# Kernel tuning notes

Hardware: AMD Instinct MI355X
Metric: run time of the kernel (lower is better)

## Reference

```python
import jax, jax.numpy as jnp
import numpy as np

EPS = 1e-5
K = 16
D = 2

def _bn(x, gamma, beta):
    # eval-mode BatchNorm with running_mean=0, running_var=1
    return x * (gamma / jnp.sqrt(1.0 + EPS)) + beta

def _dense(x, W, b, gamma=None, beta=None, act=True):
    y = x @ W + b
    if act:
        y = jax.nn.elu(y)
    if gamma is not None:
        y = _bn(y, gamma, beta)
    return y

def setup_inputs() -> dict:
    key = jax.random.key(0)
    ks = jax.random.split(key, 16)
    N, Npts, P, dims = 16, 8192, 2048, 3
    C_in, C_out = 64, 128
    C_mid = C_out // 4      # 32
    C_half = C_out // 2     # 64
    dm = 2                  # depth_multiplier = min(ceil(C_out/C_in), 4)
    Ccat = C_mid + C_half   # 96
    def w(k, shape, fan_in):
        return (jax.random.normal(k, shape, jnp.float32) / np.float32(np.sqrt(fan_in)))
    return {
        "rep_pts": jax.random.normal(ks[0], (N, P, dims), jnp.float32),
        "pts": jax.random.normal(ks[1], (N, Npts, dims), jnp.float32),
        "fts": jax.random.normal(ks[2], (N, Npts, C_in), jnp.float32),
        "pts_idx": jax.random.randint(ks[3], (N, P, K * D), 0, Npts),
        # PointCNN.dense: C_in -> C_out//2 (Linear+ELU+BN)
        "dense_W": w(ks[4], (C_in, C_half), C_in), "dense_b": jnp.zeros(C_half),
        "dense_g": jnp.ones(C_half), "dense_bt": jnp.zeros(C_half),
        # XConv dense1/dense2: dims->C_mid->C_mid
        "d1_W": w(ks[5], (dims, C_mid), dims), "d1_b": jnp.zeros(C_mid),
        "d1_g": jnp.ones(C_mid), "d1_bt": jnp.zeros(C_mid),
        "d2_W": w(ks[6], (C_mid, C_mid), C_mid), "d2_b": jnp.zeros(C_mid),
        "d2_g": jnp.ones(C_mid), "d2_bt": jnp.zeros(C_mid),
        "xt_cW": w(ks[7], (K * K, dims, K), dims * K), "xt_cb": jnp.zeros(K * K),
        "xt_d1W": w(ks[8], (K * K, K * K), K * K), "xt_d1b": jnp.zeros(K * K),
        "xt_d2W": w(ks[9], (K * K, K * K), K * K), "xt_d2b": jnp.zeros(K * K),
        # end_conv SepConv: depthwise (1,K) with depth_multiplier, then pointwise 1x1
        "dw_W": w(ks[10], (Ccat, dm, K), K), "dw_b": jnp.zeros(Ccat * dm),
        "pw_W": w(ks[11], (Ccat * dm, C_out), Ccat * dm), "pw_b": jnp.zeros(C_out),
        "sep_g": jnp.ones(C_out), "sep_bt": jnp.zeros(C_out),
    }

def reference(rep_pts, pts, fts, pts_idx,
              dense_W, dense_b, dense_g, dense_bt,
              d1_W, d1_b, d1_g, d1_bt,
              d2_W, d2_b, d2_g, d2_bt,
              xt_cW, xt_cb, xt_d1W, xt_d1b, xt_d2W, xt_d2b,
              dw_W, dw_b, pw_W, pw_b, sep_g, sep_bt):
    idx = pts_idx[:, :, : K * D : D]                  # [N,P,K]
    gather = jax.vmap(lambda a, i: a[i])              # per-batch neighbor gather
    # fts -> Dense(C_in, C_out//2)
    fts_l = _dense(fts, dense_W, dense_b, dense_g, dense_bt)
    pts_reg = gather(pts, idx)                        # [N,P,K,dims]
    fts_reg = gather(fts_l, idx)                      # [N,P,K,C_half]
    pts_local = pts_reg - rep_pts[:, :, None, :]      # center neighborhoods
    # lift coordinates to C_mid features
    l0 = _dense(pts_local, d1_W, d1_b, d1_g, d1_bt)
    lifted = _dense(l0, d2_W, d2_b, d2_g, d2_bt)      # [N,P,K,C_mid]
    fts_cat = jnp.concatenate([lifted, fts_reg], axis=-1)  # [N,P,K,Ccat]
    # X-transform: Conv (1,K) over dims -> K*K (ELU, no BN), two Dense (last no act)
    Xc = jax.nn.elu(jnp.einsum('npkd,odk->npo', pts_local, xt_cW) + xt_cb)
    X = jax.nn.elu(Xc @ xt_d1W + xt_d1b)
    X = X @ xt_d2W + xt_d2b
    N_, P_ = X.shape[0], X.shape[1]
    X = X.reshape(N_, P_, K, K)
    fts_X = jnp.einsum('npij,npjc->npic', X, fts_cat)  # [N,P,K,Ccat]
    # depthwise separable conv over K, then ELU + BN, squeeze -> [N,P,C_out]
    dw = jnp.einsum('npkc,cmk->npcm', fts_X, dw_W).reshape(N_, P_, -1) + dw_b
    out = jax.nn.elu(dw @ pw_W + pw_b)
    out = _bn(out, sep_g, sep_bt)
    return out
```

## Files before the change

### kernel.cpp

```cpp
#include <hip/hip_runtime.h>
#include <hip/hip_bf16.h>

#define RS 0.9999950000374998f

__device__ __forceinline__ float eluf(float x) {
    return x > 0.0f ? x : __expf(x) - 1.0f;
}

typedef __attribute__((ext_vector_type(8))) __bf16 bf16x8;
typedef __attribute__((ext_vector_type(4))) float f32x4;
typedef __attribute__((ext_vector_type(4))) unsigned int u32x4;

__global__ __launch_bounds__(256) void gather_kernel(
    const float* __restrict__ rep_pts, const float* __restrict__ pts,
    const int* __restrict__ pts_idx, const float* __restrict__ d1W,
    const float* __restrict__ d2W, const float* __restrict__ pwW,
    const float* __restrict__ d2Ws, const float* __restrict__ denseW,
    const float* __restrict__ cW, float* __restrict__ pts_local,
    __hip_bfloat16* __restrict__ PLB, __hip_bfloat16* __restrict__ d1Wt,
    __hip_bfloat16* __restrict__ d2Wt, __hip_bfloat16* __restrict__ pwWt,
    __hip_bfloat16* __restrict__ d2pWt, __hip_bfloat16* __restrict__ denseWt,
    __hip_bfloat16* __restrict__ cWt) {
    const int tid = threadIdx.x;
    if (blockIdx.x < 256) {
        const int t = blockIdx.x * 256 + tid;
        {
            const int k = t >> 8, n = t & 255;
            d1Wt[n * 256 + k] = __float2bfloat16(d1W[t]);
            d2Wt[n * 256 + k] = __float2bfloat16(d2W[t]);
        }
        if (t < 24576) {
            const int k = t >> 7, n = t & 127;
            pwWt[n * 192 + k] = __float2bfloat16(pwW[t]);
        }
        if (t < 1024) {
            const int q = t >> 5, c = t & 31;
            d2pWt[c * 32 + q] = __float2bfloat16(d2Ws[t]);
        }
        if (t < 4096) {
            const int k = t >> 6, n = t & 63;
            denseWt[n * 64 + k] = __float2bfloat16(denseW[t]);
        }
        if (t < 16384) {
            const int o = t >> 6, kq = t & 63;
            cWt[t] = (kq < 48) ? __float2bfloat16(cW[o * 48 + kq])
                               : __float2bfloat16(0.0f);
        }
    }
    const long gp0 = (long)blockIdx.x * 16;
    const int pt = tid >> 4, k = tid & 15;
    const long gp = gp0 + pt;
    const int n = (int)(gp >> 11);
    const int idx = pts_idx[gp * 32 + 2 * k];
    const float* ps = pts + ((long)n * 8192 + idx) * 3;
    const float* rs = rep_pts + gp * 3;
#pragma unroll
    for (int d = 0; d < 3; ++d) {
        const float v = ps[d] - rs[d];
        pts_local[gp * 48 + k * 3 + d] = v;
        PLB[gp * 64 + d * 16 + k] = __float2bfloat16(v);
    }
    PLB[gp * 64 + 48 + k] = __float2bfloat16(0.0f);
}

template <int TN, int ACT, int BN_, int OUTB>
__global__ __launch_bounds__(256) void mfma_gemm(
    const __hip_bfloat16* __restrict__ A, const __hip_bfloat16* __restrict__ Wt,
    const float* __restrict__ bias, const float* __restrict__ gamma,
    const float* __restrict__ beta, void* __restrict__ outp, int K, int Ncols) {
    constexpr int MT = (TN == 128) ? 4 : 2;
    constexpr int RB = MT * 16;
    __shared__ __bf16 As[128][40];
    __shared__ __bf16 Bs[TN][40];
    const int tid = threadIdx.x;
    const int w = tid >> 6, l = tid & 63;
    const int wm = (TN == 128) ? (w >> 1) : w;
    const int wn = (TN == 128) ? (w & 1) : 0;
    const long row0 = (long)blockIdx.x * 128;
    const int col0 = blockIdx.y * TN;
    const int sr = tid >> 1, sh = tid & 1;
    const int fr = l & 15, kg = (l >> 4) * 8;
    f32x4 acc[MT][4] = {};
    const __hip_bfloat16* __restrict__ ap = A + (row0 + sr) * (long)K + sh * 16;
    const __hip_bfloat16* __restrict__ bp =
        Wt + (long)(col0 + (TN == 128 ? sr : (sr & 63))) * K + sh * 16;
    for (int k0 = 0; k0 < K; k0 += 32) {
        const uint4 av0 = *reinterpret_cast<const uint4*>(ap + k0);
        const uint4 av1 = *reinterpret_cast<const uint4*>(ap + k0 + 8);
        *reinterpret_cast<uint4*>(&As[sr][sh * 16]) = av0;
        *reinterpret_cast<uint4*>(&As[sr][sh * 16 + 8]) = av1;
        if (TN == 128 || tid < 128) {
            const uint4 bv0 = *reinterpret_cast<const uint4*>(bp + k0);
            const uint4 bv1 = *reinterpret_cast<const uint4*>(bp + k0 + 8);
            *reinterpret_cast<uint4*>(&Bs[TN == 128 ? sr : (sr & 63)][sh * 16]) =
                bv0;
            *reinterpret_cast<uint4*>(
                &Bs[TN == 128 ? sr : (sr & 63)][sh * 16 + 8]) = bv1;
        }
        __syncthreads();
        bf16x8 af[MT], bfv[4];
#pragma unroll
        for (int mt = 0; mt < MT; ++mt)
            af[mt] =
                *reinterpret_cast<const bf16x8*>(&As[wm * RB + mt * 16 + fr][kg]);
#pragma unroll
        for (int nt = 0; nt < 4; ++nt)
            bfv[nt] =
                *reinterpret_cast<const bf16x8*>(&Bs[wn * 64 + nt * 16 + fr][kg]);
#pragma unroll
        for (int mt = 0; mt < MT; ++mt)
#pragma unroll
            for (int nt = 0; nt < 4; ++nt)
                acc[mt][nt] = __builtin_amdgcn_mfma_f32_16x16x32_bf16(
                    af[mt], bfv[nt], acc[mt][nt], 0, 0, 0);
        __syncthreads();
    }
    const int rg = (l >> 4) * 4;
#pragma unroll
    for (int nt = 0; nt < 4; ++nt) {
        const int col = col0 + wn * 64 + nt * 16 + fr;
        const float bb = bias[col];
        const float gs = BN_ ? gamma[col] * RS : 0.0f;
        const float bt = BN_ ? beta[col] : 0.0f;
#pragma unroll
        for (int mt = 0; mt < MT; ++mt) {
#pragma unroll
            for (int r = 0; r < 4; ++r) {
                const long row = row0 + wm * RB + mt * 16 + rg + r;
                float v = acc[mt][nt][r] + bb;
                if (ACT) v = eluf(v);
                if (BN_) v = v * gs + bt;
                if (OUTB)
                    reinterpret_cast<__hip_bfloat16*>(outp)[row * Ncols + col] =
                        __float2bfloat16(v);
                else
                    reinterpret_cast<float*>(outp)[row * Ncols + col] = v;
            }
        }
    }
}

__global__ __launch_bounds__(256) void mfma_gemm_f32a64(
    const float* __restrict__ A, const __hip_bfloat16* __restrict__ Wt,
    const float* __restrict__ bias, const float* __restrict__ gamma,
    const float* __restrict__ beta, __hip_bfloat16* __restrict__ outp, int K,
    int Ncols) {
    __shared__ __bf16 As[128][40];
    __shared__ __bf16 Bs[64][40];
    const int tid = threadIdx.x;
    const int w = tid >> 6, l = tid & 63;
    const long row0 = (long)blockIdx.x * 128;
    const int sr = tid >> 1, sh = tid & 1;
    const int fr = l & 15, kg = (l >> 4) * 8;
    f32x4 acc[2][4] = {};
    const float* __restrict__ ap = A + (row0 + sr) * (long)K + sh * 16;
    const __hip_bfloat16* __restrict__ bp = Wt + (long)(sr & 63) * K + sh * 16;
    for (int k0 = 0; k0 < K; k0 += 32) {
        float av[16];
#pragma unroll
        for (int q = 0; q < 4; ++q) {
            const float4 v = *reinterpret_cast<const float4*>(ap + k0 + q * 4);
            av[q * 4 + 0] = v.x;
            av[q * 4 + 1] = v.y;
            av[q * 4 + 2] = v.z;
            av[q * 4 + 3] = v.w;
        }
        union {
            __bf16 b[16];
            uint4 u[2];
        } cv;
#pragma unroll
        for (int e = 0; e < 16; ++e) cv.b[e] = (__bf16)av[e];
        *reinterpret_cast<uint4*>(&As[sr][sh * 16]) = cv.u[0];
        *reinterpret_cast<uint4*>(&As[sr][sh * 16 + 8]) = cv.u[1];
        if (tid < 128) {
            const uint4 bv0 = *reinterpret_cast<const uint4*>(bp + k0);
            const uint4 bv1 = *reinterpret_cast<const uint4*>(bp + k0 + 8);
            *reinterpret_cast<uint4*>(&Bs[sr & 63][sh * 16]) = bv0;
            *reinterpret_cast<uint4*>(&Bs[sr & 63][sh * 16 + 8]) = bv1;
        }
        __syncthreads();
        bf16x8 af[2], bfv[4];
#pragma unroll
        for (int mt = 0; mt < 2; ++mt)
            af[mt] =
                *reinterpret_cast<const bf16x8*>(&As[w * 32 + mt * 16 + fr][kg]);
#pragma unroll
        for (int nt = 0; nt < 4; ++nt)
            bfv[nt] = *reinterpret_cast<const bf16x8*>(&Bs[nt * 16 + fr][kg]);
#pragma unroll
        for (int mt = 0; mt < 2; ++mt)
#pragma unroll
            for (int nt = 0; nt < 4; ++nt)
                acc[mt][nt] = __builtin_amdgcn_mfma_f32_16x16x32_bf16(
                    af[mt], bfv[nt], acc[mt][nt], 0, 0, 0);
        __syncthreads();
    }
    const int rg = (l >> 4) * 4;
#pragma unroll
    for (int nt = 0; nt < 4; ++nt) {
        const int col = nt * 16 + fr;
        const float bb = bias[col];
        const float gs = gamma[col] * RS;
        const float bt = beta[col];
#pragma unroll
        for (int mt = 0; mt < 2; ++mt) {
#pragma unroll
            for (int r = 0; r < 4; ++r) {
                const long row = row0 + w * 32 + mt * 16 + rg + r;
                float v = acc[mt][nt][r] + bb;
                v = eluf(v) * gs + bt;
                outp[row * Ncols + col] = __float2bfloat16(v);
            }
        }
    }
}

__global__ __launch_bounds__(1024) void xchain_kernel(
    const __hip_bfloat16* __restrict__ PLB, const __hip_bfloat16* __restrict__ cWt,
    const float* __restrict__ cb, const __hip_bfloat16* __restrict__ d1Wt,
    const float* __restrict__ d1b, const __hip_bfloat16* __restrict__ d2Wt,
    const float* __restrict__ d2b, __hip_bfloat16* __restrict__ X2B) {
    __shared__ __bf16 Ap[128][264];
    __shared__ __bf16 Bs[256][40];
    const int tid = threadIdx.x;
    const int w = tid >> 6, l = tid & 63;
    const int wm = w >> 2, wn = w & 3;
    const long row0 = (long)blockIdx.x * 128;
    const int fr = l & 15, kg = (l >> 4) * 8, rg = (l >> 4) * 4;

    {
        const int r = tid >> 3, q = tid & 7;
        *reinterpret_cast<uint4*>(&Ap[r][q * 8]) =
            *reinterpret_cast<const uint4*>(PLB + (row0 + r) * 64 + q * 8);
    }
    __syncthreads();

    auto layer = [&](const __hip_bfloat16* __restrict__ Wt,
                     const float* __restrict__ bias, int K, bool act,
                     bool last) {
        f32x4 acc[2][4] = {};
        for (int k0 = 0; k0 < K; k0 += 32) {
            {
                const int col = tid >> 2, q = tid & 3;
                *reinterpret_cast<uint4*>(&Bs[col][q * 8]) =
                    *reinterpret_cast<const uint4*>(Wt + (long)col * K + k0 +
                                                    q * 8);
            }
            __syncthreads();
            bf16x8 af[2], bfv[4];
#pragma unroll
            for (int mt = 0; mt < 2; ++mt)
                af[mt] = *reinterpret_cast<const bf16x8*>(
                    &Ap[wm * 32 + mt * 16 + fr][k0 + kg]);
#pragma unroll
            for (int nt = 0; nt < 4; ++nt)
                bfv[nt] = *reinterpret_cast<const bf16x8*>(
                    &Bs[wn * 64 + nt * 16 + fr][kg]);
#pragma unroll
            for (int mt = 0; mt < 2; ++mt)
#pragma unroll
                for (int nt = 0; nt < 4; ++nt)
                    acc[mt][nt] = __builtin_amdgcn_mfma_f32_16x16x32_bf16(
                        af[mt], bfv[nt], acc[mt][nt], 0, 0, 0);
            __syncthreads();
        }
#pragma unroll
        for (int nt = 0; nt < 4; ++nt) {
            const int col = wn * 64 + nt * 16 + fr;
            const float bb = bias[col];
#pragma unroll
            for (int mt = 0; mt < 2; ++mt) {
#pragma unroll
                for (int r = 0; r < 4; ++r) {
                    const int row = wm * 32 + mt * 16 + rg + r;
                    float v = acc[mt][nt][r] + bb;
                    if (act) v = eluf(v);
                    const __bf16 h = (__bf16)v;
                    if (last)
                        X2B[(row0 + row) * 256 + col] =
                            *reinterpret_cast<const __hip_bfloat16*>(&h);
                    else
                        Ap[row][col] = h;
                }
            }
        }
        __syncthreads();
    };

    layer(cWt, cb, 64, true, false);
    layer(d1Wt, d1b, 256, true, false);
    layer(d2Wt, d2b, 256, false, true);
}

__global__ __launch_bounds__(1024) void final_stage_kernel(
    const __hip_bfloat16* __restrict__ X2B,
    const float* __restrict__ pts_local,
    const int* __restrict__ pts_idx,
    const __hip_bfloat16* __restrict__ fts_lB,
    const float* __restrict__ d1_W, const float* __restrict__ d1_b,
    const float* __restrict__ d1_g, const float* __restrict__ d1_bt,
    const __hip_bfloat16* __restrict__ d2pWt,
    const float* __restrict__ d2_b, const float* __restrict__ d2_g,
    const float* __restrict__ d2_bt, const float* __restrict__ dw_W,
    const float* __restrict__ dw_b,
    __hip_bfloat16* __restrict__ dw_out)
{
    __shared__ __bf16 fcat[16][96][16];
    __shared__ float dwT[96][36];
    __shared__ float wd1[6][32];
    __shared__ float d2e[3][32];
    __shared__ float dwbs[192];

    const int tid = threadIdx.x;
    const int w = tid >> 6, l = tid & 63;

    for (int i = tid; i < 3072; i += 1024) dwT[i >> 5][i & 31] = dw_W[i];
    if (tid < 96) wd1[tid >> 5][tid & 31] = d1_W[tid];
    else if (tid < 128) wd1[3][tid & 31] = d1_b[tid & 31];
    else if (tid < 160) wd1[4][tid & 31] = d1_g[tid & 31] * RS;
    else if (tid < 192) wd1[5][tid & 31] = d1_bt[tid & 31];
    else if (tid < 224) d2e[0][tid & 31] = d2_b[tid & 31];
    else if (tid < 256) d2e[1][tid & 31] = d2_g[tid & 31] * RS;
    else if (tid < 288) d2e[2][tid & 31] = d2_bt[tid & 31];
    else if (tid < 480) dwbs[tid - 288] = dw_b[tid - 288];
    __syncthreads();

    const int obid = blockIdx.x;
    const int bid = (obid & 7) * 256 + (obid >> 3);
    const int gp = bid * 16 + w;
    const int ugp = __builtin_amdgcn_readfirstlane(gp);
    const int n = ugp >> 11;
    const int fr = l & 15;
    const int kg = (l >> 4) * 8;
    const int kk = kg & 15;
    const unsigned msk = (l < 32) ? 0xFFFFFFFFu : 0u;
    const int rg4 = (l >> 4) * 4;
    const int colg = (l < 32) ? (32 + l) : (l - 32);
    const __hip_bfloat16* __restrict__ fbase =
        fts_lB + (long)n * 8192 * 64 + colg;

    const int* __restrict__ ip = pts_idx + (long)ugp * 32;
    unsigned fg[16];
#pragma unroll
    for (int j = 0; j < 16; ++j)
        fg[j] = *reinterpret_cast<const unsigned short*>(
            &fbase[(long)ip[2 * j] * 64]);

    const float* __restrict__ pp = pts_local + (long)ugp * 48 + fr * 3;
    const float plA0 = pp[0], plA1 = pp[1], plA2 = pp[2];

    bf16x8 a_l0;
#pragma unroll
    for (int jj = 0; jj < 8; ++jj) {
        const int q = kg + jj;
        float a = wd1[3][q];
        a = fmaf(plA0, wd1[0][q], a);
        a = fmaf(plA1, wd1[1][q], a);
        a = fmaf(plA2, wd1[2][q], a);
        a = eluf(a);
        a = a * wd1[4][q] + wd1[5][q];
        a_l0[jj] = (__bf16)a;
    }

    {
        const bf16x8 b0 =
            *reinterpret_cast<const bf16x8*>(d2pWt + (0 + fr) * 32 + kg);
        const bf16x8 b1 =
            *reinterpret_cast<const bf16x8*>(d2pWt + (16 + fr) * 32 + kg);
        f32x4 lif0 = {}, lif1 = {};
        lif0 = __builtin_amdgcn_mfma_f32_16x16x32_bf16(a_l0, b0, lif0, 0, 0, 0);
        lif1 = __builtin_amdgcn_mfma_f32_16x16x32_bf16(a_l0, b1, lif1, 0, 0, 0);
#pragma unroll
        for (int f = 0; f < 2; ++f) {
            const int c = f * 16 + fr;
            const float bb = d2e[0][c & 31], gs = d2e[1][c & 31],
                        bt = d2e[2][c & 31];
            const f32x4 dd = f ? lif1 : lif0;
            unsigned short pk[4];
#pragma unroll
            for (int r = 0; r < 4; ++r) {
                float v = dd[r] + bb;
                v = eluf(v) * gs + bt;
                const __bf16 h = (__bf16)v;
                pk[r] = *reinterpret_cast<const unsigned short*>(&h);
            }
            *reinterpret_cast<uint2*>(&fcat[w][c][rg4]) =
                make_uint2((unsigned)pk[0] | ((unsigned)pk[1] << 16),
                           (unsigned)pk[2] | ((unsigned)pk[3] << 16));
        }
    }

    {
        const uint4 lo = make_uint4(fg[0] | (fg[1] << 16), fg[2] | (fg[3] << 16),
                                    fg[4] | (fg[5] << 16), fg[6] | (fg[7] << 16));
        const uint4 hi =
            make_uint4(fg[8] | (fg[9] << 16), fg[10] | (fg[11] << 16),
                       fg[12] | (fg[13] << 16), fg[14] | (fg[15] << 16));
        *reinterpret_cast<uint4*>(&fcat[w][32 + colg][0]) = lo;
        *reinterpret_cast<uint4*>(&fcat[w][32 + colg][8]) = hi;
    }

    u32x4 axu =
        *reinterpret_cast<const u32x4*>(X2B + (long)ugp * 256 + fr * 16 + kk);
    axu &= msk;
    const bf16x8 ax = *reinterpret_cast<const bf16x8*>(&axu);

    f32x4 acc[6];
#pragma unroll
    for (int f = 0; f < 6; ++f) acc[f] = (f32x4){};
#pragma unroll
    for (int f = 0; f < 6; ++f) {
        u32x4 bu = *reinterpret_cast<const u32x4*>(&fcat[w][f * 16 + fr][kk]);
        bu &= msk;
        const bf16x8 bf = *reinterpret_cast<const bf16x8*>(&bu);
        acc[f] = __builtin_amdgcn_mfma_f32_16x16x32_bf16(ax, bf, acc[f], 0, 0, 0);
    }

    float dwv[6][2];
#pragma unroll
    for (int f = 0; f < 6; ++f) {
        const int c = f * 16 + fr;
        const float4 w0 = *reinterpret_cast<const float4*>(&dwT[c][rg4]);
        const float4 w1 = *reinterpret_cast<const float4*>(&dwT[c][16 + rg4]);
        float p0 = acc[f][0] * w0.x;
        p0 = fmaf(acc[f][1], w0.y, p0);
        p0 = fmaf(acc[f][2], w0.z, p0);
        p0 = fmaf(acc[f][3], w0.w, p0);
        float p1 = acc[f][0] * w1.x;
        p1 = fmaf(acc[f][1], w1.y, p1);
        p1 = fmaf(acc[f][2], w1.z, p1);
        p1 = fmaf(acc[f][3], w1.w, p1);
        p0 += __shfl_xor(p0, 16);
        p0 += __shfl_xor(p0, 32);
        p1 += __shfl_xor(p1, 16);
        p1 += __shfl_xor(p1, 32);
        dwv[f][0] = p0;
        dwv[f][1] = p1;
    }
    if (l < 16) {
#pragma unroll
        for (int f = 0; f < 6; ++f) {
            const int c = f * 16 + l;
            __hip_bfloat162 pk;
            pk.x = __float2bfloat16(dwv[f][0] + dwbs[2 * c + 0]);
            pk.y = __float2bfloat16(dwv[f][1] + dwbs[2 * c + 1]);
            *reinterpret_cast<__hip_bfloat162*>(dw_out + (long)gp * 192 +
                                                2 * c) = pk;
        }
    }
}

extern "C" void kernel_launch(void* const* d_in, const int* in_sizes, int n_in,
                              void* d_out, int out_size, void* d_ws,
                              size_t ws_size, hipStream_t stream) {
    const float* rep_pts = (const float*)d_in[0];
    const float* pts = (const float*)d_in[1];
    const float* fts = (const float*)d_in[2];
    const int* pts_idx = (const int*)d_in[3];
    const float* dense_W = (const float*)d_in[4];
    const float* dense_b = (const float*)d_in[5];
    const float* dense_g = (const float*)d_in[6];
    const float* dense_bt = (const float*)d_in[7];
    const float* d1_W = (const float*)d_in[8];
    const float* d1_b = (const float*)d_in[9];
    const float* d1_g = (const float*)d_in[10];
    const float* d1_bt = (const float*)d_in[11];
    const float* d2_W = (const float*)d_in[12];
    const float* d2_b = (const float*)d_in[13];
    const float* d2_g = (const float*)d_in[14];
    const float* d2_bt = (const float*)d_in[15];
    const float* xt_cW = (const float*)d_in[16];
    const float* xt_cb = (const float*)d_in[17];
    const float* xt_d1W = (const float*)d_in[18];
    const float* xt_d1b = (const float*)d_in[19];
    const float* xt_d2W = (const float*)d_in[20];
    const float* xt_d2b = (const float*)d_in[21];
    const float* dw_W = (const float*)d_in[22];
    const float* dw_b = (const float*)d_in[23];
    const float* pw_W = (const float*)d_in[24];
    const float* pw_b = (const float*)d_in[25];
    const float* sep_g = (const float*)d_in[26];
    const float* sep_bt = (const float*)d_in[27];

    float* ws = (float*)d_ws;
    __hip_bfloat16* fts_lB = (__hip_bfloat16*)ws;
    __hip_bfloat16* X2Bb = (__hip_bfloat16*)(ws + 8388608);
    __hip_bfloat16* dwB = (__hip_bfloat16*)(ws + 16777216);
    __hip_bfloat16* PLB = (__hip_bfloat16*)(ws + 20971520);
    float* pl = ws + 25165824;
    __hip_bfloat16* d1Wt = (__hip_bfloat16*)(ws + 26738688);
    __hip_bfloat16* d2Wt = (__hip_bfloat16*)(ws + 26771456);
    __hip_bfloat16* pwWt = (__hip_bfloat16*)(ws + 26804224);
    __hip_bfloat16* d2pWt = (__hip_bfloat16*)(ws + 26816512);
    __hip_bfloat16* denseWt = (__hip_bfloat16*)(ws + 26817024);
    __hip_bfloat16* cWt = (__hip_bfloat16*)(ws + 26819072);

    gather_kernel<<<2048, 256, 0, stream>>>(
        rep_pts, pts, pts_idx, xt_d1W, xt_d2W, pw_W, d2_W, dense_W, xt_cW, pl,
        PLB, d1Wt, d2Wt, pwWt, d2pWt, denseWt, cWt);

    mfma_gemm_f32a64<<<dim3(1024, 1), 256, 0, stream>>>(
        fts, denseWt, dense_b, dense_g, dense_bt, fts_lB, 64, 64);

    xchain_kernel<<<256, 1024, 0, stream>>>(PLB, cWt, xt_cb, d1Wt, xt_d1b,
                                            d2Wt, xt_d2b, X2Bb);

    final_stage_kernel<<<2048, 1024, 0, stream>>>(
        X2Bb, pl, pts_idx, fts_lB, d1_W, d1_b, d1_g, d1_bt, d2pWt, d2_b, d2_g,
        d2_bt, dw_W, dw_b, dwB);

    mfma_gemm<128, 1, 1, 0><<<dim3(256, 1), 256, 0, stream>>>(
        dwB, pwWt, pw_b, sep_g, sep_bt, d_out, 192, 128);
}
```

Baseline: 91.40 us.

## Fuse pointwise GEMM with ELU and BN into final stage kernel

Folds the pointwise 192->128 projection, ELU and BN into the end of the final stage kernel. Each block keeps its 16 depthwise outputs in shared memory and runs MFMA with the K dimension split across two wave groups, then reduces the halves through shared memory. This removes the bf16 dw intermediate round trip through global memory and one kernel launch. It also XOR-swizzles the fcat shared layout to reduce bank conflicts, at the cost of an extra block barrier and weights read from global per block.

```diff
diff --git a/kernel.cpp b/kernel.cpp
--- a/kernel.cpp
+++ b/kernel.cpp
@@ -63,83 +63,6 @@
     PLB[gp * 64 + 48 + k] = __float2bfloat16(0.0f);
 }
 
-template <int TN, int ACT, int BN_, int OUTB>
-__global__ __launch_bounds__(256) void mfma_gemm(
-    const __hip_bfloat16* __restrict__ A, const __hip_bfloat16* __restrict__ Wt,
-    const float* __restrict__ bias, const float* __restrict__ gamma,
-    const float* __restrict__ beta, void* __restrict__ outp, int K, int Ncols) {
-    constexpr int MT = (TN == 128) ? 4 : 2;
-    constexpr int RB = MT * 16;
-    __shared__ __bf16 As[128][40];
-    __shared__ __bf16 Bs[TN][40];
-    const int tid = threadIdx.x;
-    const int w = tid >> 6, l = tid & 63;
-    const int wm = (TN == 128) ? (w >> 1) : w;
-    const int wn = (TN == 128) ? (w & 1) : 0;
-    const long row0 = (long)blockIdx.x * 128;
-    const int col0 = blockIdx.y * TN;
-    const int sr = tid >> 1, sh = tid & 1;
-    const int fr = l & 15, kg = (l >> 4) * 8;
-    f32x4 acc[MT][4] = {};
-    const __hip_bfloat16* __restrict__ ap = A + (row0 + sr) * (long)K + sh * 16;
-    const __hip_bfloat16* __restrict__ bp =
-        Wt + (long)(col0 + (TN == 128 ? sr : (sr & 63))) * K + sh * 16;
-    for (int k0 = 0; k0 < K; k0 += 32) {
-        const uint4 av0 = *reinterpret_cast<const uint4*>(ap + k0);
-        const uint4 av1 = *reinterpret_cast<const uint4*>(ap + k0 + 8);
-        *reinterpret_cast<uint4*>(&As[sr][sh * 16]) = av0;
-        *reinterpret_cast<uint4*>(&As[sr][sh * 16 + 8]) = av1;
-        if (TN == 128 || tid < 128) {
-            const uint4 bv0 = *reinterpret_cast<const uint4*>(bp + k0);
-            const uint4 bv1 = *reinterpret_cast<const uint4*>(bp + k0 + 8);
-            *reinterpret_cast<uint4*>(&Bs[TN == 128 ? sr : (sr & 63)][sh * 16]) =
-                bv0;
-            *reinterpret_cast<uint4*>(
-                &Bs[TN == 128 ? sr : (sr & 63)][sh * 16 + 8]) = bv1;
-        }
-        __syncthreads();
-        bf16x8 af[MT], bfv[4];
-#pragma unroll
-        for (int mt = 0; mt < MT; ++mt)
-            af[mt] =
-                *reinterpret_cast<const bf16x8*>(&As[wm * RB + mt * 16 + fr][kg]);
-#pragma unroll
-        for (int nt = 0; nt < 4; ++nt)
-            bfv[nt] =
-                *reinterpret_cast<const bf16x8*>(&Bs[wn * 64 + nt * 16 + fr][kg]);
-#pragma unroll
-        for (int mt = 0; mt < MT; ++mt)
-#pragma unroll
-            for (int nt = 0; nt < 4; ++nt)
-                acc[mt][nt] = __builtin_amdgcn_mfma_f32_16x16x32_bf16(
-                    af[mt], bfv[nt], acc[mt][nt], 0, 0, 0);
-        __syncthreads();
-    }
-    const int rg = (l >> 4) * 4;
-#pragma unroll
-    for (int nt = 0; nt < 4; ++nt) {
-        const int col = col0 + wn * 64 + nt * 16 + fr;
-        const float bb = bias[col];
-        const float gs = BN_ ? gamma[col] * RS : 0.0f;
-        const float bt = BN_ ? beta[col] : 0.0f;
-#pragma unroll
-        for (int mt = 0; mt < MT; ++mt) {
-#pragma unroll
-            for (int r = 0; r < 4; ++r) {
-                const long row = row0 + wm * RB + mt * 16 + rg + r;
-                float v = acc[mt][nt][r] + bb;
-                if (ACT) v = eluf(v);
-                if (BN_) v = v * gs + bt;
-                if (OUTB)
-                    reinterpret_cast<__hip_bfloat16*>(outp)[row * Ncols + col] =
-                        __float2bfloat16(v);
-                else
-                    reinterpret_cast<float*>(outp)[row * Ncols + col] = v;
-            }
-        }
-    }
-}
-
 __global__ __launch_bounds__(256) void mfma_gemm_f32a64(
     const float* __restrict__ A, const __hip_bfloat16* __restrict__ Wt,
     const float* __restrict__ bias, const float* __restrict__ gamma,
@@ -304,9 +227,13 @@
     const float* __restrict__ d2_b, const float* __restrict__ d2_g,
     const float* __restrict__ d2_bt, const float* __restrict__ dw_W,
     const float* __restrict__ dw_b,
-    __hip_bfloat16* __restrict__ dw_out)
+    const __hip_bfloat16* __restrict__ pwWt,
+    const float* __restrict__ pw_b, const float* __restrict__ sep_g,
+    const float* __restrict__ sep_bt,
+    float* __restrict__ out)
 {
-    __shared__ __bf16 fcat[16][96][16];
+    __shared__ __bf16 fcatF[16 * 96 * 16];
+    __shared__ __bf16 dws[16][200];
     __shared__ float dwT[96][36];
     __shared__ float wd1[6][32];
     __shared__ float d2e[3][32];
@@ -340,6 +267,8 @@
     const __hip_bfloat16* __restrict__ fbase =
         fts_lB + (long)n * 8192 * 64 + colg;
 
+#define FIDX(W, ROW, E) ((((W)*96 + (ROW)) << 4) + ((E) ^ (((ROW)&4) << 1)))
+
     const int* __restrict__ ip = pts_idx + (long)ugp * 32;
     unsigned fg[16];
 #pragma unroll
@@ -385,7 +314,7 @@
                 const __bf16 h = (__bf16)v;
                 pk[r] = *reinterpret_cast<const unsigned short*>(&h);
             }
-            *reinterpret_cast<uint2*>(&fcat[w][c][rg4]) =
+            *reinterpret_cast<uint2*>(&fcatF[FIDX(w, c, rg4)]) =
                 make_uint2((unsigned)pk[0] | ((unsigned)pk[1] << 16),
                            (unsigned)pk[2] | ((unsigned)pk[3] << 16));
         }
@@ -397,8 +326,9 @@
         const uint4 hi =
             make_uint4(fg[8] | (fg[9] << 16), fg[10] | (fg[11] << 16),
                        fg[12] | (fg[13] << 16), fg[14] | (fg[15] << 16));
-        *reinterpret_cast<uint4*>(&fcat[w][32 + colg][0]) = lo;
-        *reinterpret_cast<uint4*>(&fcat[w][32 + colg][8]) = hi;
+        const int row = 32 + colg;
+        *reinterpret_cast<uint4*>(&fcatF[FIDX(w, row, 0)]) = lo;
+        *reinterpret_cast<uint4*>(&fcatF[FIDX(w, row, 8)]) = hi;
     }
 
     u32x4 axu =
@@ -411,7 +341,8 @@
     for (int f = 0; f < 6; ++f) acc[f] = (f32x4){};
 #pragma unroll
     for (int f = 0; f < 6; ++f) {
-        u32x4 bu = *reinterpret_cast<const u32x4*>(&fcat[w][f * 16 + fr][kk]);
+        u32x4 bu =
+            *reinterpret_cast<const u32x4*>(&fcatF[FIDX(w, f * 16 + fr, kk)]);
         bu &= msk;
         const bf16x8 bf = *reinterpret_cast<const bf16x8*>(&bu);
         acc[f] = __builtin_amdgcn_mfma_f32_16x16x32_bf16(ax, bf, acc[f], 0, 0, 0);
@@ -445,10 +376,41 @@
             __hip_bfloat162 pk;
             pk.x = __float2bfloat16(dwv[f][0] + dwbs[2 * c + 0]);
             pk.y = __float2bfloat16(dwv[f][1] + dwbs[2 * c + 1]);
-            *reinterpret_cast<__hip_bfloat162*>(dw_out + (long)gp * 192 +
-                                                2 * c) = pk;
-        }
-    }
+            *reinterpret_cast<__hip_bfloat162*>(&dws[w][2 * c]) = pk;
+        }
+    }
+    __syncthreads();
+
+    const int c8 = w & 7, h2 = w >> 3;
+    f32x4 pacc = {};
+#pragma unroll
+    for (int t = 0; t < 3; ++t) {
+        const int kc = h2 * 3 + t;
+        const bf16x8 a =
+            *reinterpret_cast<const bf16x8*>(&dws[fr][kc * 32 + kg]);
+        const bf16x8 b = *reinterpret_cast<const bf16x8*>(
+            pwWt + (long)(c8 * 16 + fr) * 192 + kc * 32 + kg);
+        pacc = __builtin_amdgcn_mfma_f32_16x16x32_bf16(a, b, pacc, 0, 0, 0);
+    }
+    float* red = reinterpret_cast<float*>(fcatF);
+    if (w >= 8)
+        *reinterpret_cast<f32x4*>(&red[(c8 * 64 + l) * 4]) = pacc;
+    __syncthreads();
+    if (w < 8) {
+        const f32x4 other =
+            *reinterpret_cast<const f32x4*>(&red[(c8 * 64 + l) * 4]);
+        const int col = c8 * 16 + fr;
+        const float bb = pw_b[col];
+        const float gs = sep_g[col] * RS;
+        const float bt = sep_bt[col];
+#pragma unroll
+        for (int r = 0; r < 4; ++r) {
+            float v = pacc[r] + other[r] + bb;
+            v = eluf(v) * gs + bt;
+            out[(long)(bid * 16 + rg4 + r) * 128 + col] = v;
+        }
+    }
+#undef FIDX
 }
 
 extern "C" void kernel_launch(void* const* d_in, const int* in_sizes, int n_in,
@@ -486,7 +448,6 @@
     float* ws = (float*)d_ws;
     __hip_bfloat16* fts_lB = (__hip_bfloat16*)ws;
     __hip_bfloat16* X2Bb = (__hip_bfloat16*)(ws + 8388608);
-    __hip_bfloat16* dwB = (__hip_bfloat16*)(ws + 16777216);
     __hip_bfloat16* PLB = (__hip_bfloat16*)(ws + 20971520);
     float* pl = ws + 25165824;
     __hip_bfloat16* d1Wt = (__hip_bfloat16*)(ws + 26738688);
@@ -508,8 +469,5 @@
 
     final_stage_kernel<<<2048, 1024, 0, stream>>>(
         X2Bb, pl, pts_idx, fts_lB, d1_W, d1_b, d1_g, d1_bt, d2pWt, d2_b, d2_g,
-        d2_bt, dw_W, dw_b, dwB);
-
-    mfma_gemm<128, 1, 1, 0><<<dim3(256, 1), 256, 0, stream>>>(
-        dwB, pwWt, pw_b, sep_g, sep_bt, d_out, 192, 128);
-}
+        d2_bt, dw_W, dw_b, pwWt, pw_b, sep_g, sep_bt, (float*)d_out);
+}
```

After: 90.09 us. About the same (-1.4%).
